# Optimization experiments

Measured on AMD Instinct MI355X. Metric: run time of the kernel, lower is better.

Reference implementation:

```python
import jax, jax.numpy as jnp
import numpy as np

B, N, C = 8, 4096, 512
NUM_HEADS = 8
HEAD_DIM = C // NUM_HEADS
POS_RES = 32  # only table with res <= max_resolution=32


def _interp_linear(pos, out_len):
    # F.interpolate(mode='linear', align_corners=False) along the length axis (axis 1)
    in_len = pos.shape[1]
    scale = in_len / out_len
    coords = (jnp.arange(out_len, dtype=jnp.float32) + 0.5) * scale - 0.5
    coords = jnp.clip(coords, 0.0, in_len - 1)
    i0 = jnp.floor(coords).astype(jnp.int32)
    i1 = jnp.minimum(i0 + 1, in_len - 1)
    w = (coords - i0.astype(jnp.float32))[None, :, None]
    return pos[:, i0, :] * (1.0 - w) + pos[:, i1, :] * w


def setup_inputs():
    key = jax.random.key(0)
    k = jax.random.split(key, 4)
    x = jax.random.normal(k[0], (B, N, C), jnp.float32)
    pos_32 = jax.random.normal(k[1], (1, POS_RES ** 3, C), jnp.float32)  # torch.randn init
    s = 1.0 / np.sqrt(C)
    w_qkv = jax.random.normal(k[2], (C, 3 * C), jnp.float32) * s
    b_qkv = jnp.zeros((3 * C,), jnp.float32)
    w_proj = jax.random.normal(k[3], (C, C), jnp.float32) * s
    b_proj = jnp.zeros((C,), jnp.float32)
    return {"x": x, "pos_32": pos_32, "w_qkv": w_qkv, "b_qkv": b_qkv,
            "w_proj": w_proj, "b_proj": b_proj, "resolution": 16}


def reference(x, pos_32, w_qkv, b_qkv, w_proj, b_proj, resolution):
    Bx, Nx, Cx = x.shape
    target_len = resolution ** 3  # 4096 -> nearest table pos_32 is interpolated down
    pos = pos_32 if pos_32.shape[1] == target_len else _interp_linear(pos_32, target_len)
    if pos.shape[1] == Nx:
        x = x + pos
    qkv = (x @ w_qkv + b_qkv).reshape(Bx, Nx, 3, NUM_HEADS, HEAD_DIM)
    q, k, v = qkv[:, :, 0], qkv[:, :, 1], qkv[:, :, 2]  # each [B, N, H, D]
    # Faithful to source: q,k,v are NOT permuted to [B,H,N,D], so q @ k.T
    # contracts head_dim per token, yielding [B, N, H, H] head-axis attention.
    attn = jnp.einsum('bnid,bnjd->bnij', q, k) / np.sqrt(HEAD_DIM)
    attn = jax.nn.softmax(attn, axis=-1)
    out = jnp.einsum('bnij,bnjd->bnid', attn, v)  # [B, N, H, D]
    # torch: .transpose(1, 2).reshape(B, N, C) -> flatten of [B, H, N, D]
    out = jnp.transpose(out, (0, 2, 1, 3)).reshape(Bx, Nx, Cx)
    return out @ w_proj + b_proj
```

## Files before the change

### kernel.cpp

```cpp
#include <hip/hip_runtime.h>
#include <hip/hip_bf16.h>

using bf16 = __hip_bfloat16;
typedef __attribute__((ext_vector_type(8))) short short8;
typedef __attribute__((ext_vector_type(4))) float f32x4;

#define AS1U(p) ((const __attribute__((address_space(1))) unsigned int*)(p))
#define AS3U(p) ((__attribute__((address_space(3))) unsigned int*)(p))

__device__ __forceinline__ float bflo(unsigned u) { return __uint_as_float(u << 16); }
__device__ __forceinline__ float bfhi(unsigned u) { return __uint_as_float(u & 0xffff0000u); }
__device__ __forceinline__ unsigned short f2bf(float f) {
    union { float f; unsigned u; } v{f};
    unsigned r = v.u + 0x7fffu + ((v.u >> 16) & 1u);
    return (unsigned short)(r >> 16);
}

__global__ __launch_bounds__(256) void kprep(const float* __restrict__ wq,
                                             const float* __restrict__ wp,
                                             const float* __restrict__ x,
                                             const float* __restrict__ pos,
                                             bf16* __restrict__ wqT,
                                             bf16* __restrict__ wpT,
                                             bf16* __restrict__ xp) {
    int bid = blockIdx.x;
    __shared__ float t[32][33];
    if (bid < 1024) {
        const float* in; bf16* out; int Cc, bx, by;
        if (bid < 768) { in = wq; out = wqT; Cc = 1536; bx = bid % 48; by = bid / 48; }
        else { int i = bid - 768; in = wp; out = wpT; Cc = 512; bx = i & 15; by = i >> 4; }
        const int R = 512;
        int tx = threadIdx.x & 31, ty = threadIdx.x >> 5;
        int c0 = bx * 32, r0 = by * 32;
#pragma unroll
        for (int i = 0; i < 4; ++i)
            t[ty + i * 8][tx] = in[(size_t)(r0 + ty + i * 8) * Cc + c0 + tx];
        __syncthreads();
#pragma unroll
        for (int i = 0; i < 4; ++i)
            out[(size_t)(c0 + ty + i * 8) * R + r0 + tx] = __float2bfloat16(t[tx][ty + i * 8]);
    } else {
        size_t idx4 = (size_t)(bid - 1024) * 256 + threadIdx.x;
        size_t e = idx4 * 4;
        int c = (int)(e & 511);
        size_t m = e >> 9;
        int n = (int)(m & 4095);
        float4 xv = *(const float4*)(x + e);
        float4 p3 = *(const float4*)(pos + (size_t)(n * 8 + 3) * 512 + c);
        float4 p4 = *(const float4*)(pos + (size_t)(n * 8 + 4) * 512 + c);
        unsigned r[2];
        float v0 = xv.x + 0.5f * (p3.x + p4.x);
        float v1 = xv.y + 0.5f * (p3.y + p4.y);
        float v2 = xv.z + 0.5f * (p3.z + p4.z);
        float v3 = xv.w + 0.5f * (p3.w + p4.w);
        r[0] = (unsigned)f2bf(v0) | ((unsigned)f2bf(v1) << 16);
        r[1] = (unsigned)f2bf(v2) | ((unsigned)f2bf(v3) << 16);
        *(uint2*)(xp + e) = *(uint2*)r;
    }
}

template <typename OutT>
__global__ __launch_bounds__(256) void kgemm_lds(const bf16* __restrict__ A,
                                                 const bf16* __restrict__ Bt,
                                                 const float* __restrict__ bias,
                                                 OutT* __restrict__ C,
                                                 int M, int N, int K) {
    constexpr int BM = 128, BN = 128, BK = 32;
    __shared__ bf16 As[BM * BK];
    __shared__ bf16 Bs[BN * BK];
    const int tid = threadIdx.x;
    const int lane = tid & 63, wave = tid >> 6;
    const int wr = wave >> 1, wc = wave & 1;
    const int ntn = N / 128;
    const int nwg = gridDim.x;
    const int bid = blockIdx.x;
    const int swz = (bid & 7) * (nwg >> 3) + (bid >> 3);
    const int bm = (swz / ntn) * BM;
    const int bn = (swz % ntn) * BN;

    const int c0 = wave * 128 + lane;
    const int c1 = c0 + 64;
    const int r0 = c0 >> 2, o0 = (c0 & 3) * 8;
    const int r1 = c1 >> 2, o1 = (c1 & 3) * 8;
    char* ldsA0 = (char*)As + wave * 2048;
    char* ldsB0 = (char*)Bs + wave * 2048;

    const bf16* a0 = A + (size_t)(bm + r0) * K + o0;
    const bf16* a1 = A + (size_t)(bm + r1) * K + o1;
    const bf16* b0 = Bt + (size_t)(bn + r0) * K + o0;
    const bf16* b1 = Bt + (size_t)(bn + r1) * K + o1;

    f32x4 acc[4][4];
#pragma unroll
    for (int i = 0; i < 4; ++i)
#pragma unroll
        for (int j = 0; j < 4; ++j) acc[i][j] = f32x4{0.f, 0.f, 0.f, 0.f};

    const int fr = lane & 15;
    const int fk = (lane >> 4) * 8;
    const bf16* arow = As + (wr * 64 + fr) * BK + fk;
    const bf16* brow = Bs + (wc * 64 + fr) * BK + fk;

    for (int k0 = 0; k0 < K; k0 += BK) {
        if (k0) __syncthreads();
        __builtin_amdgcn_global_load_lds(AS1U(a0 + k0), AS3U(ldsA0), 16, 0, 0);
        __builtin_amdgcn_global_load_lds(AS1U(a1 + k0), AS3U(ldsA0 + 1024), 16, 0, 0);
        __builtin_amdgcn_global_load_lds(AS1U(b0 + k0), AS3U(ldsB0), 16, 0, 0);
        __builtin_amdgcn_global_load_lds(AS1U(b1 + k0), AS3U(ldsB0 + 1024), 16, 0, 0);
        __syncthreads();
        short8 af[4], bf_[4];
#pragma unroll
        for (int mi = 0; mi < 4; ++mi)
            af[mi] = *(const short8*)(arow + mi * 16 * BK);
#pragma unroll
        for (int nj = 0; nj < 4; ++nj)
            bf_[nj] = *(const short8*)(brow + nj * 16 * BK);
#pragma unroll
        for (int mi = 0; mi < 4; ++mi)
#pragma unroll
            for (int nj = 0; nj < 4; ++nj)
                acc[mi][nj] = __builtin_amdgcn_mfma_f32_16x16x32_bf16(af[mi], bf_[nj], acc[mi][nj], 0, 0, 0);
    }

#pragma unroll
    for (int mi = 0; mi < 4; ++mi) {
#pragma unroll
        for (int nj = 0; nj < 4; ++nj) {
            int col = bn + wc * 64 + nj * 16 + fr;
            int row0 = bm + wr * 64 + mi * 16 + (lane >> 4) * 4;
            float bv = bias[col];
#pragma unroll
            for (int r = 0; r < 4; ++r) {
                float val = acc[mi][nj][r] + bv;
                if constexpr (sizeof(OutT) == 2)
                    C[(size_t)(row0 + r) * N + col] = (OutT)__float2bfloat16(val);
                else
                    C[(size_t)(row0 + r) * N + col] = (OutT)val;
            }
        }
    }
}

__global__ __launch_bounds__(256) void kattn(const bf16* __restrict__ qkv,
                                             bf16* __restrict__ oscr) {
    int T = blockIdx.x * 256 + threadIdx.x;
    int token = T >> 3, head = T & 7;
    int b = token >> 12, n = token & 4095;
    const bf16* row = qkv + (size_t)token * 1536;

    uint4 qp[8];
#pragma unroll
    for (int c = 0; c < 8; ++c) qp[c] = *(const uint4*)(row + head * 64 + c * 8);

    float s[8];
#pragma unroll
    for (int j = 0; j < 8; ++j) {
        float acc = 0.f;
#pragma unroll
        for (int c = 0; c < 8; ++c) {
            uint4 kp = *(const uint4*)(row + 512 + j * 64 + c * 8);
            const unsigned* ku = &kp.x; const unsigned* qu = &qp[c].x;
#pragma unroll
            for (int w = 0; w < 4; ++w) {
                acc = fmaf(bflo(qu[w]), bflo(ku[w]), acc);
                acc = fmaf(bfhi(qu[w]), bfhi(ku[w]), acc);
            }
        }
        s[j] = acc * 0.125f;
    }
    float mx = s[0];
#pragma unroll
    for (int j = 1; j < 8; ++j) mx = fmaxf(mx, s[j]);
    float sum = 0.f;
#pragma unroll
    for (int j = 0; j < 8; ++j) { s[j] = __expf(s[j] - mx); sum += s[j]; }
    float inv = 1.f / sum;
#pragma unroll
    for (int j = 0; j < 8; ++j) s[j] *= inv;

    float o[64];
#pragma unroll
    for (int d = 0; d < 64; ++d) o[d] = 0.f;
#pragma unroll
    for (int j = 0; j < 8; ++j) {
        float pj = s[j];
#pragma unroll
        for (int c = 0; c < 8; ++c) {
            uint4 vp = *(const uint4*)(row + 1024 + j * 64 + c * 8);
            const unsigned* vu = &vp.x;
#pragma unroll
            for (int w = 0; w < 4; ++w) {
                o[c * 8 + w * 2]     = fmaf(pj, bflo(vu[w]), o[c * 8 + w * 2]);
                o[c * 8 + w * 2 + 1] = fmaf(pj, bfhi(vu[w]), o[c * 8 + w * 2 + 1]);
            }
        }
    }
    size_t orow = (size_t)b * 4096 + head * 512 + (n >> 3);
    bf16* op = oscr + orow * 512 + (n & 7) * 64;
#pragma unroll
    for (int c = 0; c < 8; ++c) {
        unsigned rr[4];
#pragma unroll
        for (int w = 0; w < 4; ++w)
            rr[w] = (unsigned)f2bf(o[c * 8 + w * 2]) | ((unsigned)f2bf(o[c * 8 + w * 2 + 1]) << 16);
        *(uint4*)(op + c * 8) = *(uint4*)rr;
    }
}

extern "C" void kernel_launch(void* const* d_in, const int* in_sizes, int n_in,
                              void* d_out, int out_size, void* d_ws, size_t ws_size,
                              hipStream_t stream) {
    const float* x      = (const float*)d_in[0];
    const float* pos32  = (const float*)d_in[1];
    const float* w_qkv  = (const float*)d_in[2];
    const float* b_qkv  = (const float*)d_in[3];
    const float* w_proj = (const float*)d_in[4];
    const float* b_proj = (const float*)d_in[5];

    char* ws = (char*)d_ws;
    bf16* xp   = (bf16*)(ws);
    bf16* qkv  = (bf16*)(ws + 33554432);
    bf16* wqT  = (bf16*)(ws + 134217728);
    bf16* wpT  = (bf16*)(ws + 135790592);
    bf16* ascr = xp;

    kprep<<<17408, 256, 0, stream>>>(w_qkv, w_proj, x, pos32, wqT, wpT, xp);
    kgemm_lds<bf16><<<256 * 12, 256, 0, stream>>>(xp, wqT, b_qkv, qkv, 32768, 1536, 512);
    kattn<<<1024, 256, 0, stream>>>(qkv, ascr);
    kgemm_lds<float><<<256 * 4, 256, 0, stream>>>(ascr, wpT, b_proj, (float*)d_out, 32768, 512, 512);
}
```

Baseline: 159.2 us.

## Replace GEMM with 256x256-tile, 8-wave, double-buffered LDS pipelined kernel

Both GEMMs now use a new kernel built on 256x256 output tiles, 512 threads, and BK=64 K-steps. Each step is staged into double-buffered LDS with direct global-to-LDS loads, an XOR swizzle to avoid bank conflicts, and explicit vmcnt waits, so the next tile loads while MFMAs run. The larger tiles raise data reuse per global byte, and s_setprio is used to favour the MFMA waves. In exchange the kernel needs 128 KB of LDS per block, which limits occupancy. The K loop is hard-coded to 8 steps, so it only works for K=512.

```diff
diff --git a/kernel.cpp b/kernel.cpp
--- a/kernel.cpp
+++ b/kernel.cpp
@@ -60,82 +60,114 @@
 }
 
 template <typename OutT>
-__global__ __launch_bounds__(256) void kgemm_lds(const bf16* __restrict__ A,
+__global__ __launch_bounds__(512, 2) void kgemm8(const bf16* __restrict__ A,
                                                  const bf16* __restrict__ Bt,
                                                  const float* __restrict__ bias,
                                                  OutT* __restrict__ C,
                                                  int M, int N, int K) {
-    constexpr int BM = 128, BN = 128, BK = 32;
-    __shared__ bf16 As[BM * BK];
-    __shared__ bf16 Bs[BN * BK];
+    __shared__ __align__(16) char smem[131072];
     const int tid = threadIdx.x;
     const int lane = tid & 63, wave = tid >> 6;
-    const int wr = wave >> 1, wc = wave & 1;
-    const int ntn = N / 128;
+    const int wm = wave >> 2, wn = wave & 3;
+    const int fr = lane & 15;
+    const int lo16 = (lane >> 4) * 16;
+    const int lo16s = lo16 ^ (((fr >> 2) & 1) << 5);
+
+    const int ntn = N >> 8;
     const int nwg = gridDim.x;
     const int bid = blockIdx.x;
     const int swz = (bid & 7) * (nwg >> 3) + (bid >> 3);
-    const int bm = (swz / ntn) * BM;
-    const int bn = (swz % ntn) * BN;
-
-    const int c0 = wave * 128 + lane;
-    const int c1 = c0 + 64;
-    const int r0 = c0 >> 2, o0 = (c0 & 3) * 8;
-    const int r1 = c1 >> 2, o1 = (c1 & 3) * 8;
-    char* ldsA0 = (char*)As + wave * 2048;
-    char* ldsB0 = (char*)Bs + wave * 2048;
-
-    const bf16* a0 = A + (size_t)(bm + r0) * K + o0;
-    const bf16* a1 = A + (size_t)(bm + r1) * K + o1;
-    const bf16* b0 = Bt + (size_t)(bn + r0) * K + o0;
-    const bf16* b1 = Bt + (size_t)(bn + r1) * K + o1;
-
-    f32x4 acc[4][4];
-#pragma unroll
-    for (int i = 0; i < 4; ++i)
+    const int bm = (swz / ntn) << 8;
+    const int bn = (swz % ntn) << 8;
+
+    const int lp = lane ^ (((lane >> 5) & 1) << 1);
+    const int r = wave * 8 + (lp >> 3);
+    const int o = (lp & 7) * 8;
+    const bf16* srcA[4]; const bf16* srcB[4];
+#pragma unroll
+    for (int h = 0; h < 2; ++h)
+#pragma unroll
+        for (int jj = 0; jj < 2; ++jj) {
+            srcA[h * 2 + jj] = A  + (size_t)(bm + h * 128 + jj * 64 + r) * K + o;
+            srcB[h * 2 + jj] = Bt + (size_t)(bn + h * 128 + jj * 64 + r) * K + o;
+        }
+
+    const char* pAb[2]; const char* pBb[2];
+#pragma unroll
+    for (int b = 0; b < 2; ++b) {
+        pAb[b] = smem + b * 65536 + wm * 16384 + fr * 128 + lo16s;
+        pBb[b] = smem + b * 65536 + 32768 + (wn >> 1) * 16384 + (wn & 1) * 8192 + fr * 128 + lo16s;
+    }
+
+    f32x4 acc[8][4];
+#pragma unroll
+    for (int i = 0; i < 8; ++i)
 #pragma unroll
         for (int j = 0; j < 4; ++j) acc[i][j] = f32x4{0.f, 0.f, 0.f, 0.f};
 
-    const int fr = lane & 15;
-    const int fk = (lane >> 4) * 8;
-    const bf16* arow = As + (wr * 64 + fr) * BK + fk;
-    const bf16* brow = Bs + (wc * 64 + fr) * BK + fk;
-
-    for (int k0 = 0; k0 < K; k0 += BK) {
-        if (k0) __syncthreads();
-        __builtin_amdgcn_global_load_lds(AS1U(a0 + k0), AS3U(ldsA0), 16, 0, 0);
-        __builtin_amdgcn_global_load_lds(AS1U(a1 + k0), AS3U(ldsA0 + 1024), 16, 0, 0);
-        __builtin_amdgcn_global_load_lds(AS1U(b0 + k0), AS3U(ldsB0), 16, 0, 0);
-        __builtin_amdgcn_global_load_lds(AS1U(b1 + k0), AS3U(ldsB0 + 1024), 16, 0, 0);
-        __syncthreads();
-        short8 af[4], bf_[4];
-#pragma unroll
-        for (int mi = 0; mi < 4; ++mi)
-            af[mi] = *(const short8*)(arow + mi * 16 * BK);
-#pragma unroll
-        for (int nj = 0; nj < 4; ++nj)
-            bf_[nj] = *(const short8*)(brow + nj * 16 * BK);
-#pragma unroll
-        for (int mi = 0; mi < 4; ++mi)
-#pragma unroll
-            for (int nj = 0; nj < 4; ++nj)
-                acc[mi][nj] = __builtin_amdgcn_mfma_f32_16x16x32_bf16(af[mi], bf_[nj], acc[mi][nj], 0, 0, 0);
-    }
-
-#pragma unroll
-    for (int mi = 0; mi < 4; ++mi) {
+    auto stage = [&](int kt, int b) {
+        char* base = smem + b * 65536;
+#pragma unroll
+        for (int i = 0; i < 4; ++i) {
+            const int off = (i >> 1) * 16384 + (i & 1) * 8192 + wave * 1024;
+            __builtin_amdgcn_global_load_lds(AS1U(srcA[i] + kt * 64), AS3U(base + off), 16, 0, 0);
+            __builtin_amdgcn_global_load_lds(AS1U(srcB[i] + kt * 64), AS3U(base + 32768 + off), 16, 0, 0);
+        }
+    };
+
+    stage(0, 0);
+    stage(1, 1);
+
+#pragma unroll
+    for (int t = 0; t < 8; ++t) {
+        const int b = t & 1;
+        if (t < 7) asm volatile("s_waitcnt vmcnt(8)" ::: "memory");
+        else       asm volatile("s_waitcnt vmcnt(0)" ::: "memory");
+        __builtin_amdgcn_s_barrier();
+        __builtin_amdgcn_sched_barrier(0);
+        const char* pA = pAb[b];
+        const char* pB = pBb[b];
+#pragma unroll
+        for (int kk = 0; kk < 2; ++kk) {
+            short8 af[8];
+#pragma unroll
+            for (int mi = 0; mi < 8; ++mi)
+                af[mi] = *(const short8*)(pA + mi * 2048 + kk * 64);
+#pragma unroll
+            for (int njh = 0; njh < 2; ++njh) {
+                short8 bfr[2];
+#pragma unroll
+                for (int j = 0; j < 2; ++j)
+                    bfr[j] = *(const short8*)(pB + (njh * 2 + j) * 2048 + kk * 64);
+                __builtin_amdgcn_s_setprio(1);
+#pragma unroll
+                for (int mi = 0; mi < 8; ++mi)
+#pragma unroll
+                    for (int j = 0; j < 2; ++j)
+                        acc[mi][njh * 2 + j] = __builtin_amdgcn_mfma_f32_16x16x32_bf16(
+                            af[mi], bfr[j], acc[mi][njh * 2 + j], 0, 0, 0);
+                __builtin_amdgcn_s_setprio(0);
+            }
+        }
+        __builtin_amdgcn_sched_barrier(0);
+        __builtin_amdgcn_s_barrier();
+        if (t < 6) stage(t + 2, b);
+    }
+
+#pragma unroll
+    for (int mi = 0; mi < 8; ++mi) {
 #pragma unroll
         for (int nj = 0; nj < 4; ++nj) {
-            int col = bn + wc * 64 + nj * 16 + fr;
-            int row0 = bm + wr * 64 + mi * 16 + (lane >> 4) * 4;
+            int col = bn + wn * 64 + nj * 16 + fr;
+            int row0 = bm + wm * 128 + mi * 16 + (lane >> 4) * 4;
             float bv = bias[col];
 #pragma unroll
-            for (int r = 0; r < 4; ++r) {
-                float val = acc[mi][nj][r] + bv;
+            for (int rr = 0; rr < 4; ++rr) {
+                float val = acc[mi][nj][rr] + bv;
                 if constexpr (sizeof(OutT) == 2)
-                    C[(size_t)(row0 + r) * N + col] = (OutT)__float2bfloat16(val);
+                    C[(size_t)(row0 + rr) * N + col] = (OutT)__float2bfloat16(val);
                 else
-                    C[(size_t)(row0 + r) * N + col] = (OutT)val;
+                    C[(size_t)(row0 + rr) * N + col] = (OutT)val;
             }
         }
     }
@@ -225,7 +257,7 @@
     bf16* ascr = xp;
 
     kprep<<<17408, 256, 0, stream>>>(w_qkv, w_proj, x, pos32, wqT, wpT, xp);
-    kgemm_lds<bf16><<<256 * 12, 256, 0, stream>>>(xp, wqT, b_qkv, qkv, 32768, 1536, 512);
+    kgemm8<bf16><<<768, 512, 0, stream>>>(xp, wqT, b_qkv, qkv, 32768, 1536, 512);
     kattn<<<1024, 256, 0, stream>>>(qkv, ascr);
-    kgemm_lds<float><<<256 * 4, 256, 0, stream>>>(ascr, wpT, b_proj, (float*)d_out, 32768, 512, 512);
-}
+    kgemm8<float><<<256, 512, 0, stream>>>(ascr, wpT, b_proj, (float*)d_out, 32768, 512, 512);
+}
```

After: 152.8 us. -4.0%, faster.
